# Performance work log

Hardware: AMD Instinct MI355X
Metric: run time of the kernel (lower is better)

## Reference

```python
import jax, jax.numpy as jnp
import numpy as np

NUM_POSITIONS = 4096
EMBED_DIM = 512
BSZ, SEQ_LEN = 16, 4096


def setup_inputs() -> dict:
    key = jax.random.key(0)
    k1, k2 = jax.random.split(key)
    input_tensor = jax.random.normal(k1, (BSZ, SEQ_LEN, EMBED_DIM), dtype=jnp.float32)
    pv = jax.random.normal(k2, (NUM_POSITIONS, EMBED_DIM), dtype=jnp.float32)
    # L2-normalize each position vector (as in _init_position_vectors)
    pv = pv / jnp.linalg.norm(pv, axis=1, keepdims=True)
    return {"input_tensor": input_tensor, "position_vectors": pv}


def reference(input_tensor, position_vectors):
    # input_tensor: [B, S, D]; position_vectors: [P, D] with S <= P.
    seq_len, d = input_tensor.shape[1], input_tensor.shape[-1]
    pos = position_vectors[:seq_len]  # [S, D]
    # Batched circular convolution over the last axis via rFFT.
    x_fft = jnp.fft.rfft(input_tensor, axis=-1)          # [B, S, D//2+1] complex
    p_fft = jnp.fft.rfft(pos, axis=-1)[None, :, :]       # [1, S, D//2+1]
    out = jnp.fft.irfft(x_fft * p_fft, n=d, axis=-1)     # [B, S, D]
    return out.astype(input_tensor.dtype)
```

## Files before the change

### kernel.cpp

```cpp
#include <hip/hip_runtime.h>
#include <math.h>

#ifndef M_PI
#define M_PI 3.14159265358979323846
#endif

#define BSZ 16
#define SEQ 4096
#define DIM 512

#define REG_SZ 656

__device__ __forceinline__ void wsync(){
  asm volatile("s_waitcnt lgkmcnt(0)" ::: "memory");
  __builtin_amdgcn_wave_barrier();
}

__device__ __forceinline__ float2 cadd(float2 a, float2 b){ return make_float2(a.x+b.x, a.y+b.y); }
__device__ __forceinline__ float2 csub(float2 a, float2 b){ return make_float2(a.x-b.x, a.y-b.y); }
__device__ __forceinline__ float2 cmul(float2 a, float2 b){
  return make_float2(fmaf(a.x, b.x, -(a.y*b.y)), fmaf(a.x, b.y, a.y*b.x));
}
__device__ __forceinline__ float2 cmulc(float2 a, float2 b){
  return make_float2(fmaf(a.x, b.x, a.y*b.y), fmaf(a.y, b.x, -(a.x*b.y)));
}
__device__ __forceinline__ float2 mul_mi(float2 a){ return make_float2(a.y, -a.x); }

__device__ __forceinline__ void dft8(const float2* in, float2* out){
  float2 t0 = cadd(in[0], in[4]), t1 = csub(in[0], in[4]);
  float2 t2 = cadd(in[2], in[6]), t3 = csub(in[2], in[6]);
  float2 E0 = cadd(t0, t2), E2 = csub(t0, t2);
  float2 m3 = mul_mi(t3);
  float2 E1 = cadd(t1, m3), E3 = csub(t1, m3);
  float2 s0 = cadd(in[1], in[5]), s1 = csub(in[1], in[5]);
  float2 s2 = cadd(in[3], in[7]), s3 = csub(in[3], in[7]);
  float2 O0 = cadd(s0, s2), O2 = csub(s0, s2);
  float2 n3 = mul_mi(s3);
  float2 O1 = cadd(s1, n3), O3 = csub(s1, n3);
  const float C = 0.70710678118654752440f;
  float2 w1o = make_float2(C*(O1.x + O1.y), C*(O1.y - O1.x));
  float2 w2o = mul_mi(O2);
  float2 w3o = make_float2(C*(O3.y - O3.x), -(C*(O3.x + O3.y)));
  out[0] = cadd(E0, O0); out[4] = csub(E0, O0);
  out[1] = cadd(E1, w1o); out[5] = csub(E1, w1o);
  out[2] = cadd(E2, w2o); out[6] = csub(E2, w2o);
  out[3] = cadd(E3, w3o); out[7] = csub(E3, w3o);
}

__device__ __forceinline__ void idft8(const float2* in, float2* out){
  float2 t[8];
  dft8(in, t);
  out[0]=t[0]; out[1]=t[7]; out[2]=t[6]; out[3]=t[5];
  out[4]=t[4]; out[5]=t[3]; out[6]=t[2]; out[7]=t[1];
}

__device__ __forceinline__ void fft512_fwd(float2* v, float2* lds, int lane,
                                           const float2* wA, const float2* wB){
  const int a = lane >> 3, b = lane & 7;
  float2 t[8];
  dft8(v, t);
  #pragma unroll
  for (int r = 1; r < 8; ++r) t[r] = cmul(t[r], wA[r]);
  wsync();
  #pragma unroll
  for (int r = 0; r < 8; ++r) lds[72*r + lane] = t[r];
  wsync();
  #pragma unroll
  for (int j2 = 0; j2 < 8; ++j2) v[j2] = lds[72*a + b + 8*j2];
  dft8(v, t);
  #pragma unroll
  for (int r2 = 1; r2 < 8; ++r2) t[r2] = cmul(t[r2], wB[r2]);
  wsync();
  #pragma unroll
  for (int r2 = 0; r2 < 8; ++r2) lds[a + 82*r2 + 10*b] = t[r2];
  wsync();
  #pragma unroll
  for (int i2 = 0; i2 < 8; ++i2) v[i2] = lds[a + 82*b + 10*i2];
  dft8(v, t);
  #pragma unroll
  for (int m = 0; m < 8; ++m) v[m] = t[m];
}

__device__ __forceinline__ void fft512_inv(float2* v, float2* lds, int lane,
                                           const float2* wA, const float2* wB){
  const int a = lane >> 3, b = lane & 7;
  float2 t[8];
  idft8(v, t);
  wsync();
  #pragma unroll
  for (int i2 = 0; i2 < 8; ++i2) lds[a + 82*b + 10*i2] = t[i2];
  wsync();
  #pragma unroll
  for (int r2 = 0; r2 < 8; ++r2) v[r2] = lds[a + 82*r2 + 10*b];
  #pragma unroll
  for (int r2 = 1; r2 < 8; ++r2) v[r2] = cmulc(v[r2], wB[r2]);
  idft8(v, t);
  wsync();
  #pragma unroll
  for (int j2 = 0; j2 < 8; ++j2) lds[72*a + b + 8*j2] = t[j2];
  wsync();
  #pragma unroll
  for (int r = 0; r < 8; ++r) v[r] = lds[72*r + lane];
  #pragma unroll
  for (int r = 1; r < 8; ++r) v[r] = cmulc(v[r], wA[r]);
  idft8(v, t);
  #pragma unroll
  for (int j = 0; j < 8; ++j) v[j] = t[j];
}

__global__ void __launch_bounds__(256)
circconv_kernel(const float* __restrict__ x, const float* __restrict__ p,
                float* __restrict__ out){
  __shared__ float2 lds_all[4 * REG_SZ];
  const int lane = threadIdx.x & 63;
  const int wid  = threadIdx.x >> 6;
  float2* lds = lds_all + wid * REG_SZ;

  const int g    = blockIdx.x * 4 + wid;
  const int s    = g >> 1;
  const int half = g & 1;
  const int b    = lane & 7;

  float pr[8];
  {
    const float* prow = p + (size_t)s * DIM;
    #pragma unroll
    for (int j = 0; j < 8; ++j) pr[j] = prow[lane + 64*j];
  }

  const int b_lo = half * 8;
  const size_t row_stride = (size_t)SEQ * DIM;
  size_t pf_base0 = ((size_t)b_lo * SEQ + s) * DIM;
  size_t pf_base1 = pf_base0 + row_stride;
  float r0[8], r1[8];
  #pragma unroll
  for (int j = 0; j < 8; ++j){
    r0[j] = x[pf_base0 + lane + 64*j];
    r1[j] = x[pf_base1 + lane + 64*j];
  }

  float2 wA[8], wB[8];
  wA[0] = make_float2(1.f, 0.f); wB[0] = make_float2(1.f, 0.f);
  #pragma unroll
  for (int r = 1; r < 8; ++r){
    float sv, cv;
    sincosf(-2.0f*(float)M_PI*(float)(lane*r)*(1.0f/512.0f), &sv, &cv);
    wA[r] = make_float2(cv, sv);
    sincosf(-2.0f*(float)M_PI*(float)(b*r)*(1.0f/64.0f), &sv, &cv);
    wB[r] = make_float2(cv, sv);
  }

  float2 pf[8];
  #pragma unroll
  for (int j = 0; j < 8; ++j) pf[j] = make_float2(pr[j], 0.f);
  fft512_fwd(pf, lds, lane, wA, wB);
  #pragma unroll
  for (int m = 0; m < 8; ++m){ pf[m].x *= (1.0f/512.0f); pf[m].y *= (1.0f/512.0f); }

  for (int pi = 0; pi < 4; ++pi){
    const size_t cb0 = ((size_t)(b_lo + 2*pi) * SEQ + s) * DIM;
    const size_t cb1 = cb0 + row_stride;

    float2 v[8];
    #pragma unroll
    for (int j = 0; j < 8; ++j) v[j] = make_float2(r0[j], r1[j]);

    if (pi < 3){
      const size_t nb0 = cb0 + 2*row_stride;
      const size_t nb1 = nb0 + row_stride;
      #pragma unroll
      for (int j = 0; j < 8; ++j){
        r0[j] = x[nb0 + lane + 64*j];
        r1[j] = x[nb1 + lane + 64*j];
      }
    }

    fft512_fwd(v, lds, lane, wA, wB);
    #pragma unroll
    for (int m = 0; m < 8; ++m) v[m] = cmul(v[m], pf[m]);
    fft512_inv(v, lds, lane, wA, wB);
    #pragma unroll
    for (int j = 0; j < 8; ++j){
      out[cb0 + lane + 64*j] = v[j].x;
      out[cb1 + lane + 64*j] = v[j].y;
    }
  }
}

extern "C" void kernel_launch(void* const* d_in, const int* in_sizes, int n_in,
                              void* d_out, int out_size, void* d_ws, size_t ws_size,
                              hipStream_t stream) {
  (void)in_sizes; (void)n_in; (void)d_ws; (void)ws_size; (void)out_size;
  const float* x  = (const float*)d_in[0];
  const float* p  = (const float*)d_in[1];
  float* o        = (float*)d_out;
  circconv_kernel<<<SEQ*2/4, 256, 0, stream>>>(x, p, o);
}
```

Baseline: 248.1 us.

## Precompute position spectra in separate kernel and batch two FFTs per wave

Position-vector FFTs now run once in a prepass kernel that writes the spectra to workspace, so the main kernel stops recomputing them for each half-batch group. The main kernel processes two packed complex FFTs (four rows) at once per wave and drops the software prefetch. Blocks shrink to 128 threads with a launch_bounds occupancy hint. Twiddles come from one sincos plus recurrence instead of seven sincos calls. This adds a workspace round trip and a second launch, and the larger per-thread register footprint may reduce occupancy.

```diff
diff --git a/kernel.cpp b/kernel.cpp
--- a/kernel.cpp
+++ b/kernel.cpp
@@ -5,7 +5,6 @@
 #define M_PI 3.14159265358979323846
 #endif
 
-#define BSZ 16
 #define SEQ 4096
 #define DIM 512
 
@@ -54,6 +53,20 @@
   out[4]=t[4]; out[5]=t[3]; out[6]=t[2]; out[7]=t[1];
 }
 
+__device__ __forceinline__ void make_twiddles(int lane, float2* wA, float2* wB){
+  const int b = lane & 7;
+  float sv, cv;
+  sincosf(-2.0f*(float)M_PI*(float)lane*(1.0f/512.0f), &sv, &cv);
+  const float2 a1 = make_float2(cv, sv);
+  sincosf(-2.0f*(float)M_PI*(float)b*(1.0f/64.0f), &sv, &cv);
+  const float2 b1 = make_float2(cv, sv);
+  wA[0] = make_float2(1.f, 0.f); wB[0] = make_float2(1.f, 0.f);
+  wA[1] = a1; wB[1] = b1;
+  #pragma unroll
+  for (int r = 2; r < 8; ++r){ wA[r] = cmul(wA[r-1], a1); wB[r] = cmul(wB[r-1], b1); }
+}
+
+
 __device__ __forceinline__ void fft512_fwd(float2* v, float2* lds, int lane,
                                            const float2* wA, const float2* wB){
   const int a = lane >> 3, b = lane & 7;
@@ -81,108 +94,142 @@
   for (int m = 0; m < 8; ++m) v[m] = t[m];
 }
 
-__device__ __forceinline__ void fft512_inv(float2* v, float2* lds, int lane,
-                                           const float2* wA, const float2* wB){
+__device__ __forceinline__ void fft512_fwd2(float2* vA, float2* vB,
+                                            float2* ldsA, float2* ldsB, int lane,
+                                            const float2* wA, const float2* wB){
   const int a = lane >> 3, b = lane & 7;
-  float2 t[8];
-  idft8(v, t);
-  wsync();
-  #pragma unroll
-  for (int i2 = 0; i2 < 8; ++i2) lds[a + 82*b + 10*i2] = t[i2];
-  wsync();
-  #pragma unroll
-  for (int r2 = 0; r2 < 8; ++r2) v[r2] = lds[a + 82*r2 + 10*b];
-  #pragma unroll
-  for (int r2 = 1; r2 < 8; ++r2) v[r2] = cmulc(v[r2], wB[r2]);
-  idft8(v, t);
-  wsync();
-  #pragma unroll
-  for (int j2 = 0; j2 < 8; ++j2) lds[72*a + b + 8*j2] = t[j2];
-  wsync();
-  #pragma unroll
-  for (int r = 0; r < 8; ++r) v[r] = lds[72*r + lane];
-  #pragma unroll
-  for (int r = 1; r < 8; ++r) v[r] = cmulc(v[r], wA[r]);
-  idft8(v, t);
-  #pragma unroll
-  for (int j = 0; j < 8; ++j) v[j] = t[j];
+  float2 tA[8], tB[8];
+  dft8(vA, tA); dft8(vB, tB);
+  #pragma unroll
+  for (int r = 1; r < 8; ++r){ tA[r] = cmul(tA[r], wA[r]); tB[r] = cmul(tB[r], wA[r]); }
+  wsync();
+  #pragma unroll
+  for (int r = 0; r < 8; ++r){ ldsA[72*r + lane] = tA[r]; ldsB[72*r + lane] = tB[r]; }
+  wsync();
+  #pragma unroll
+  for (int j2 = 0; j2 < 8; ++j2){ vA[j2] = ldsA[72*a + b + 8*j2]; vB[j2] = ldsB[72*a + b + 8*j2]; }
+  dft8(vA, tA); dft8(vB, tB);
+  #pragma unroll
+  for (int r2 = 1; r2 < 8; ++r2){ tA[r2] = cmul(tA[r2], wB[r2]); tB[r2] = cmul(tB[r2], wB[r2]); }
+  wsync();
+  #pragma unroll
+  for (int r2 = 0; r2 < 8; ++r2){ ldsA[a + 82*r2 + 10*b] = tA[r2]; ldsB[a + 82*r2 + 10*b] = tB[r2]; }
+  wsync();
+  #pragma unroll
+  for (int i2 = 0; i2 < 8; ++i2){ vA[i2] = ldsA[a + 82*b + 10*i2]; vB[i2] = ldsB[a + 82*b + 10*i2]; }
+  dft8(vA, tA); dft8(vB, tB);
+  #pragma unroll
+  for (int m = 0; m < 8; ++m){ vA[m] = tA[m]; vB[m] = tB[m]; }
+}
+
+__device__ __forceinline__ void fft512_inv2(float2* vA, float2* vB,
+                                            float2* ldsA, float2* ldsB, int lane,
+                                            const float2* wA, const float2* wB){
+  const int a = lane >> 3, b = lane & 7;
+  float2 tA[8], tB[8];
+  idft8(vA, tA); idft8(vB, tB);
+  wsync();
+  #pragma unroll
+  for (int i2 = 0; i2 < 8; ++i2){ ldsA[a + 82*b + 10*i2] = tA[i2]; ldsB[a + 82*b + 10*i2] = tB[i2]; }
+  wsync();
+  #pragma unroll
+  for (int r2 = 0; r2 < 8; ++r2){ vA[r2] = ldsA[a + 82*r2 + 10*b]; vB[r2] = ldsB[a + 82*r2 + 10*b]; }
+  #pragma unroll
+  for (int r2 = 1; r2 < 8; ++r2){ vA[r2] = cmulc(vA[r2], wB[r2]); vB[r2] = cmulc(vB[r2], wB[r2]); }
+  idft8(vA, tA); idft8(vB, tB);
+  wsync();
+  #pragma unroll
+  for (int j2 = 0; j2 < 8; ++j2){ ldsA[72*a + b + 8*j2] = tA[j2]; ldsB[72*a + b + 8*j2] = tB[j2]; }
+  wsync();
+  #pragma unroll
+  for (int r = 0; r < 8; ++r){ vA[r] = ldsA[72*r + lane]; vB[r] = ldsB[72*r + lane]; }
+  #pragma unroll
+  for (int r = 1; r < 8; ++r){ vA[r] = cmulc(vA[r], wA[r]); vB[r] = cmulc(vB[r], wA[r]); }
+  idft8(vA, tA); idft8(vB, tB);
+  #pragma unroll
+  for (int j = 0; j < 8; ++j){ vA[j] = tA[j]; vB[j] = tB[j]; }
 }
 
 __global__ void __launch_bounds__(256)
-circconv_kernel(const float* __restrict__ x, const float* __restrict__ p,
-                float* __restrict__ out){
+pfft_kernel(const float* __restrict__ p, float2* __restrict__ pspec){
   __shared__ float2 lds_all[4 * REG_SZ];
   const int lane = threadIdx.x & 63;
   const int wid  = threadIdx.x >> 6;
   float2* lds = lds_all + wid * REG_SZ;
-
-  const int g    = blockIdx.x * 4 + wid;
+  const int s = blockIdx.x * 4 + wid;
+
+  float2 wA[8], wB[8];
+  make_twiddles(lane, wA, wB);
+
+  const float* prow = p + (size_t)s * DIM;
+  float2 pf[8];
+  #pragma unroll
+  for (int j = 0; j < 8; ++j) pf[j] = make_float2(prow[lane + 64*j], 0.f);
+  fft512_fwd(pf, lds, lane, wA, wB);
+  #pragma unroll
+  for (int m = 0; m < 8; ++m){
+    pf[m].x *= (1.0f/512.0f); pf[m].y *= (1.0f/512.0f);
+    pspec[(size_t)s * DIM + 64*m + lane] = pf[m];
+  }
+}
+
+__global__ void __launch_bounds__(128, 3)
+circconv_kernel(const float* __restrict__ x, const float* __restrict__ p,
+                const float2* __restrict__ pspec, float* __restrict__ out){
+  __shared__ float2 lds_all[2 * 2 * REG_SZ];
+  const int lane = threadIdx.x & 63;
+  const int wid  = threadIdx.x >> 6;
+  float2* ldsA = lds_all + wid * 2 * REG_SZ;
+  float2* ldsB = ldsA + REG_SZ;
+
+  const int g    = blockIdx.x * 2 + wid;
   const int s    = g >> 1;
   const int half = g & 1;
-  const int b    = lane & 7;
-
-  float pr[8];
-  {
+
+  float2 wA[8], wB[8];
+  make_twiddles(lane, wA, wB);
+
+  float2 pf[8];
+  if (pspec){
+    #pragma unroll
+    for (int m = 0; m < 8; ++m) pf[m] = pspec[(size_t)s * DIM + 64*m + lane];
+  } else {
     const float* prow = p + (size_t)s * DIM;
     #pragma unroll
-    for (int j = 0; j < 8; ++j) pr[j] = prow[lane + 64*j];
+    for (int j = 0; j < 8; ++j) pf[j] = make_float2(prow[lane + 64*j], 0.f);
+    fft512_fwd(pf, ldsA, lane, wA, wB);
+    #pragma unroll
+    for (int m = 0; m < 8; ++m){ pf[m].x *= (1.0f/512.0f); pf[m].y *= (1.0f/512.0f); }
   }
 
+  const size_t row_stride = (size_t)SEQ * DIM;
   const int b_lo = half * 8;
-  const size_t row_stride = (size_t)SEQ * DIM;
-  size_t pf_base0 = ((size_t)b_lo * SEQ + s) * DIM;
-  size_t pf_base1 = pf_base0 + row_stride;
-  float r0[8], r1[8];
-  #pragma unroll
-  for (int j = 0; j < 8; ++j){
-    r0[j] = x[pf_base0 + lane + 64*j];
-    r1[j] = x[pf_base1 + lane + 64*j];
-  }
-
-  float2 wA[8], wB[8];
-  wA[0] = make_float2(1.f, 0.f); wB[0] = make_float2(1.f, 0.f);
-  #pragma unroll
-  for (int r = 1; r < 8; ++r){
-    float sv, cv;
-    sincosf(-2.0f*(float)M_PI*(float)(lane*r)*(1.0f/512.0f), &sv, &cv);
-    wA[r] = make_float2(cv, sv);
-    sincosf(-2.0f*(float)M_PI*(float)(b*r)*(1.0f/64.0f), &sv, &cv);
-    wB[r] = make_float2(cv, sv);
-  }
-
-  float2 pf[8];
-  #pragma unroll
-  for (int j = 0; j < 8; ++j) pf[j] = make_float2(pr[j], 0.f);
-  fft512_fwd(pf, lds, lane, wA, wB);
-  #pragma unroll
-  for (int m = 0; m < 8; ++m){ pf[m].x *= (1.0f/512.0f); pf[m].y *= (1.0f/512.0f); }
-
-  for (int pi = 0; pi < 4; ++pi){
-    const size_t cb0 = ((size_t)(b_lo + 2*pi) * SEQ + s) * DIM;
-    const size_t cb1 = cb0 + row_stride;
-
-    float2 v[8];
-    #pragma unroll
-    for (int j = 0; j < 8; ++j) v[j] = make_float2(r0[j], r1[j]);
-
-    if (pi < 3){
-      const size_t nb0 = cb0 + 2*row_stride;
-      const size_t nb1 = nb0 + row_stride;
-      #pragma unroll
-      for (int j = 0; j < 8; ++j){
-        r0[j] = x[nb0 + lane + 64*j];
-        r1[j] = x[nb1 + lane + 64*j];
-      }
+
+  for (int iter = 0; iter < 2; ++iter){
+    const int r0 = b_lo + iter * 4;
+    const size_t base0 = ((size_t)r0 * SEQ + s) * DIM;
+    const size_t base1 = base0 + row_stride;
+    const size_t base2 = base0 + 2 * row_stride;
+    const size_t base3 = base0 + 3 * row_stride;
+
+    float2 vA[8], vB[8];
+    #pragma unroll
+    for (int j = 0; j < 8; ++j){
+      vA[j] = make_float2(x[base0 + lane + 64*j], x[base1 + lane + 64*j]);
+      vB[j] = make_float2(x[base2 + lane + 64*j], x[base3 + lane + 64*j]);
     }
 
-    fft512_fwd(v, lds, lane, wA, wB);
-    #pragma unroll
-    for (int m = 0; m < 8; ++m) v[m] = cmul(v[m], pf[m]);
-    fft512_inv(v, lds, lane, wA, wB);
+    fft512_fwd2(vA, vB, ldsA, ldsB, lane, wA, wB);
+    #pragma unroll
+    for (int m = 0; m < 8; ++m){ vA[m] = cmul(vA[m], pf[m]); vB[m] = cmul(vB[m], pf[m]); }
+    fft512_inv2(vA, vB, ldsA, ldsB, lane, wA, wB);
+
     #pragma unroll
     for (int j = 0; j < 8; ++j){
-      out[cb0 + lane + 64*j] = v[j].x;
-      out[cb1 + lane + 64*j] = v[j].y;
+      out[base0 + lane + 64*j] = vA[j].x;
+      out[base1 + lane + 64*j] = vA[j].y;
+      out[base2 + lane + 64*j] = vB[j].x;
+      out[base3 + lane + 64*j] = vB[j].y;
     }
   }
 }
@@ -190,9 +237,14 @@
 extern "C" void kernel_launch(void* const* d_in, const int* in_sizes, int n_in,
                               void* d_out, int out_size, void* d_ws, size_t ws_size,
                               hipStream_t stream) {
-  (void)in_sizes; (void)n_in; (void)d_ws; (void)ws_size; (void)out_size;
+  (void)in_sizes; (void)n_in; (void)out_size;
   const float* x  = (const float*)d_in[0];
   const float* p  = (const float*)d_in[1];
   float* o        = (float*)d_out;
-  circconv_kernel<<<SEQ*2/4, 256, 0, stream>>>(x, p, o);
-}
+
+  const size_t pspec_bytes = (size_t)SEQ * DIM * sizeof(float2);
+  float2* pspec = (ws_size >= pspec_bytes) ? (float2*)d_ws : nullptr;
+
+  if (pspec) pfft_kernel<<<SEQ/4, 256, 0, stream>>>(p, pspec);
+  circconv_kernel<<<SEQ*2/2, 128, 0, stream>>>(x, p, pspec, o);
+}
```

Result: slower. 309.4 us (+24.7%).

## Precompute position spectra in a separate kernel and parallelize batch pairs across waves

Applied to the files above, without the earlier changes.

Adds a pre-pass kernel that FFTs each position vector once into workspace. The main kernel then assigns one batch pair per wave instead of four sequential pairs, which multiplies the grid size fourfold and removes the duplicated position FFT. Twiddles are now built by recurrence from a single sincos rather than seven. The cost is an extra launch and a 16 MB spectrum round trip through memory, the loss of the manual register prefetch, and a fallback path used when the workspace is too small.

```diff
diff --git a/kernel.cpp b/kernel.cpp
--- a/kernel.cpp
+++ b/kernel.cpp
@@ -5,7 +5,6 @@
 #define M_PI 3.14159265358979323846
 #endif
 
-#define BSZ 16
 #define SEQ 4096
 #define DIM 512
 
@@ -54,6 +53,19 @@
   out[4]=t[4]; out[5]=t[3]; out[6]=t[2]; out[7]=t[1];
 }
 
+__device__ __forceinline__ void make_twiddles(int lane, float2* wA, float2* wB){
+  const int b = lane & 7;
+  float sv, cv;
+  sincosf(-2.0f*(float)M_PI*(float)lane*(1.0f/512.0f), &sv, &cv);
+  const float2 a1 = make_float2(cv, sv);
+  sincosf(-2.0f*(float)M_PI*(float)b*(1.0f/64.0f), &sv, &cv);
+  const float2 b1 = make_float2(cv, sv);
+  wA[0] = make_float2(1.f, 0.f); wB[0] = make_float2(1.f, 0.f);
+  wA[1] = a1; wB[1] = b1;
+  #pragma unroll
+  for (int r = 2; r < 8; ++r){ wA[r] = cmul(wA[r-1], a1); wB[r] = cmul(wB[r-1], b1); }
+}
+
 __device__ __forceinline__ void fft512_fwd(float2* v, float2* lds, int lane,
                                            const float2* wA, const float2* wB){
   const int a = lane >> 3, b = lane & 7;
@@ -109,7 +121,30 @@
 }
 
 __global__ void __launch_bounds__(256)
-circconv_kernel(const float* __restrict__ x, const float* __restrict__ p,
+pfft_kernel(const float* __restrict__ p, float2* __restrict__ pspec){
+  __shared__ float2 lds_all[4 * REG_SZ];
+  const int lane = threadIdx.x & 63;
+  const int wid  = threadIdx.x >> 6;
+  float2* lds = lds_all + wid * REG_SZ;
+  const int s = blockIdx.x * 4 + wid;
+
+  float2 wA[8], wB[8];
+  make_twiddles(lane, wA, wB);
+
+  const float* prow = p + (size_t)s * DIM;
+  float2 pf[8];
+  #pragma unroll
+  for (int j = 0; j < 8; ++j) pf[j] = make_float2(prow[lane + 64*j], 0.f);
+  fft512_fwd(pf, lds, lane, wA, wB);
+  #pragma unroll
+  for (int m = 0; m < 8; ++m){
+    pf[m].x *= (1.0f/512.0f); pf[m].y *= (1.0f/512.0f);
+    pspec[(size_t)s * DIM + 64*m + lane] = pf[m];
+  }
+}
+
+__global__ void __launch_bounds__(256)
+circconv_kernel(const float* __restrict__ x, const float2* __restrict__ pspec,
                 float* __restrict__ out){
   __shared__ float2 lds_all[4 * REG_SZ];
   const int lane = threadIdx.x & 63;
@@ -117,72 +152,85 @@
   float2* lds = lds_all + wid * REG_SZ;
 
   const int g    = blockIdx.x * 4 + wid;
+  const int s    = g >> 3;
+  const int pr   = g & 7;
+
+  const size_t row_stride = (size_t)SEQ * DIM;
+  const size_t base0 = ((size_t)(2*pr) * SEQ + s) * DIM;
+  const size_t base1 = base0 + row_stride;
+
+  float2 pf[8];
+  #pragma unroll
+  for (int m = 0; m < 8; ++m) pf[m] = pspec[(size_t)s * DIM + 64*m + lane];
+
+  float re[8], im[8];
+  #pragma unroll
+  for (int j = 0; j < 8; ++j){
+    re[j] = x[base0 + lane + 64*j];
+    im[j] = x[base1 + lane + 64*j];
+  }
+
+  float2 wA[8], wB[8];
+  make_twiddles(lane, wA, wB);
+
+  float2 v[8];
+  #pragma unroll
+  for (int j = 0; j < 8; ++j) v[j] = make_float2(re[j], im[j]);
+
+  fft512_fwd(v, lds, lane, wA, wB);
+  #pragma unroll
+  for (int m = 0; m < 8; ++m) v[m] = cmul(v[m], pf[m]);
+  fft512_inv(v, lds, lane, wA, wB);
+
+  #pragma unroll
+  for (int j = 0; j < 8; ++j){
+    out[base0 + lane + 64*j] = v[j].x;
+    out[base1 + lane + 64*j] = v[j].y;
+  }
+}
+
+__global__ void __launch_bounds__(256)
+circconv_fallback_kernel(const float* __restrict__ x, const float* __restrict__ p,
+                         float* __restrict__ out){
+  __shared__ float2 lds_all[4 * REG_SZ];
+  const int lane = threadIdx.x & 63;
+  const int wid  = threadIdx.x >> 6;
+  float2* lds = lds_all + wid * REG_SZ;
+
+  const int g    = blockIdx.x * 4 + wid;
   const int s    = g >> 1;
   const int half = g & 1;
-  const int b    = lane & 7;
-
-  float pr[8];
+
+  float2 wA[8], wB[8];
+  make_twiddles(lane, wA, wB);
+
+  float2 pf[8];
   {
     const float* prow = p + (size_t)s * DIM;
     #pragma unroll
-    for (int j = 0; j < 8; ++j) pr[j] = prow[lane + 64*j];
-  }
-
+    for (int j = 0; j < 8; ++j) pf[j] = make_float2(prow[lane + 64*j], 0.f);
+    fft512_fwd(pf, lds, lane, wA, wB);
+    #pragma unroll
+    for (int m = 0; m < 8; ++m){ pf[m].x *= (1.0f/512.0f); pf[m].y *= (1.0f/512.0f); }
+  }
+
+  const size_t row_stride = (size_t)SEQ * DIM;
   const int b_lo = half * 8;
-  const size_t row_stride = (size_t)SEQ * DIM;
-  size_t pf_base0 = ((size_t)b_lo * SEQ + s) * DIM;
-  size_t pf_base1 = pf_base0 + row_stride;
-  float r0[8], r1[8];
-  #pragma unroll
-  for (int j = 0; j < 8; ++j){
-    r0[j] = x[pf_base0 + lane + 64*j];
-    r1[j] = x[pf_base1 + lane + 64*j];
-  }
-
-  float2 wA[8], wB[8];
-  wA[0] = make_float2(1.f, 0.f); wB[0] = make_float2(1.f, 0.f);
-  #pragma unroll
-  for (int r = 1; r < 8; ++r){
-    float sv, cv;
-    sincosf(-2.0f*(float)M_PI*(float)(lane*r)*(1.0f/512.0f), &sv, &cv);
-    wA[r] = make_float2(cv, sv);
-    sincosf(-2.0f*(float)M_PI*(float)(b*r)*(1.0f/64.0f), &sv, &cv);
-    wB[r] = make_float2(cv, sv);
-  }
-
-  float2 pf[8];
-  #pragma unroll
-  for (int j = 0; j < 8; ++j) pf[j] = make_float2(pr[j], 0.f);
-  fft512_fwd(pf, lds, lane, wA, wB);
-  #pragma unroll
-  for (int m = 0; m < 8; ++m){ pf[m].x *= (1.0f/512.0f); pf[m].y *= (1.0f/512.0f); }
-
-  for (int pi = 0; pi < 4; ++pi){
-    const size_t cb0 = ((size_t)(b_lo + 2*pi) * SEQ + s) * DIM;
-    const size_t cb1 = cb0 + row_stride;
-
+  for (int bb = b_lo; bb < b_lo + 8; bb += 2){
+    const size_t base0 = ((size_t)bb * SEQ + s) * DIM;
+    const size_t base1 = base0 + row_stride;
     float2 v[8];
     #pragma unroll
-    for (int j = 0; j < 8; ++j) v[j] = make_float2(r0[j], r1[j]);
-
-    if (pi < 3){
-      const size_t nb0 = cb0 + 2*row_stride;
-      const size_t nb1 = nb0 + row_stride;
-      #pragma unroll
-      for (int j = 0; j < 8; ++j){
-        r0[j] = x[nb0 + lane + 64*j];
-        r1[j] = x[nb1 + lane + 64*j];
-      }
-    }
-
+    for (int j = 0; j < 8; ++j)
+      v[j] = make_float2(x[base0 + lane + 64*j], x[base1 + lane + 64*j]);
     fft512_fwd(v, lds, lane, wA, wB);
     #pragma unroll
     for (int m = 0; m < 8; ++m) v[m] = cmul(v[m], pf[m]);
     fft512_inv(v, lds, lane, wA, wB);
     #pragma unroll
     for (int j = 0; j < 8; ++j){
-      out[cb0 + lane + 64*j] = v[j].x;
-      out[cb1 + lane + 64*j] = v[j].y;
+      out[base0 + lane + 64*j] = v[j].x;
+      out[base1 + lane + 64*j] = v[j].y;
     }
   }
 }
@@ -190,9 +238,17 @@
 extern "C" void kernel_launch(void* const* d_in, const int* in_sizes, int n_in,
                               void* d_out, int out_size, void* d_ws, size_t ws_size,
                               hipStream_t stream) {
-  (void)in_sizes; (void)n_in; (void)d_ws; (void)ws_size; (void)out_size;
+  (void)in_sizes; (void)n_in; (void)out_size;
   const float* x  = (const float*)d_in[0];
   const float* p  = (const float*)d_in[1];
   float* o        = (float*)d_out;
-  circconv_kernel<<<SEQ*2/4, 256, 0, stream>>>(x, p, o);
-}
+
+  const size_t pspec_bytes = (size_t)SEQ * DIM * sizeof(float2);
+  if (ws_size >= pspec_bytes){
+    float2* pspec = (float2*)d_ws;
+    pfft_kernel<<<SEQ/4, 256, 0, stream>>>(p, pspec);
+    circconv_kernel<<<SEQ*8/4, 256, 0, stream>>>(x, pspec, o);
+  } else {
+    circconv_fallback_kernel<<<SEQ*2/4, 256, 0, stream>>>(x, p, o);
+  }
+}
```

Result: no change. 247.0 us (-0.4%).
